# Optimization experiments

Hardware: AMD Instinct MI355X
Metric: run time of the kernel (lower is better)

## Reference

```python
import jax, jax.numpy as jnp
from jax import lax
import numpy as np

SUB_SAMPLE = 16
NMS_THRESH = 0.7
N_PRE_NMS = 2000
N_POST_NMS = 300
MIN_SIZE = 16.0
SCALE = 1.0
NEG_INF = -1e9


def _anchor_base(base=16.0, ratios=(0.5, 1.0, 2.0), scales=(8.0, 16.0, 32.0)):
    r = np.asarray(ratios, np.float32)[:, None]
    s = np.asarray(scales, np.float32)[None, :]
    h = base * s * np.sqrt(r)
    w = base * s * np.sqrt(1.0 / r)
    ctr = base / 2.0
    ab = np.stack([ctr - h / 2, ctr - w / 2, ctr + h / 2, ctr + w / 2], axis=-1)
    return ab.reshape(-1, 4).astype(np.float32)  # [9,4] (y1,x1,y2,x2)


def _decode(anchors, locs):
    # anchors/locs: [K,4]; loc2bbox
    ah = anchors[:, 2] - anchors[:, 0]
    aw = anchors[:, 3] - anchors[:, 1]
    acy = anchors[:, 0] + 0.5 * ah
    acx = anchors[:, 1] + 0.5 * aw
    dy, dx, dh, dw = locs[:, 0], locs[:, 1], locs[:, 2], locs[:, 3]
    cy = dy * ah + acy
    cx = dx * aw + acx
    h = jnp.exp(dh) * ah
    w = jnp.exp(dw) * aw
    return jnp.stack([cy - 0.5 * h, cx - 0.5 * w, cy + 0.5 * h, cx + 0.5 * w], axis=-1)


def _pairwise_iou(b):
    # b: [P,4] y1x1y2x2
    tl = jnp.maximum(b[:, None, :2], b[None, :, :2])
    br = jnp.minimum(b[:, None, 2:], b[None, :, 2:])
    wh = jnp.clip(br - tl, 0.0)
    inter = wh[..., 0] * wh[..., 1]
    area = (b[:, 2] - b[:, 0]) * (b[:, 3] - b[:, 1])
    return inter / (area[:, None] + area[None, :] - inter + 1e-9)


def _propose(locs_i, fg_i, anchors, img_h, img_w):
    boxes = _decode(anchors, locs_i)
    boxes = jnp.stack([
        jnp.clip(boxes[:, 0], 0.0, img_h), jnp.clip(boxes[:, 1], 0.0, img_w),
        jnp.clip(boxes[:, 2], 0.0, img_h), jnp.clip(boxes[:, 3], 0.0, img_w)], axis=-1)
    hs = boxes[:, 2] - boxes[:, 0]
    ws = boxes[:, 3] - boxes[:, 1]
    ok = (hs >= MIN_SIZE * SCALE) & (ws >= MIN_SIZE * SCALE)
    sc = jnp.where(ok, fg_i, NEG_INF)
    top_sc, order = lax.top_k(sc, N_PRE_NMS)  # sorted desc by score
    b = boxes[order]
    iou = _pairwise_iou(b)
    idx = jnp.arange(N_PRE_NMS)
    sup = (iou > NMS_THRESH) & (idx[None, :] > idx[:, None])  # only suppress lower-scored
    keep0 = top_sc > NEG_INF / 2  # drop min-size-filtered padding

    def body(i, keep):
        return jnp.where(keep[i], keep & ~sup[i], keep)

    keep = lax.fori_loop(0, N_PRE_NMS, body, keep0)
    prio = jnp.where(keep, idx, N_PRE_NMS)
    sel = jnp.argsort(prio)[:N_POST_NMS]  # kept boxes first, score order preserved
    valid = keep[sel]
    rois = jnp.where(valid[:, None], b[sel], 0.0)
    return rois, valid


def setup_inputs() -> dict:
    key = jax.random.key(0)
    ks = jax.random.split(key, 6)
    N, C, Hf, Wf = 8, 512, 64, 64
    std = 0.01  # normal_init(0, 0.01)
    return {
        "x": jax.random.normal(ks[0], (N, C, Hf, Wf), jnp.float32),
        "conv1_w": jax.random.normal(ks[1], (512, 512, 3, 3), jnp.float32) * std,
        "conv1_b": jnp.zeros((512,), jnp.float32),
        "score_w": jax.random.normal(ks[2], (18, 512, 1, 1), jnp.float32) * std,
        "score_b": jnp.zeros((18,), jnp.float32),
        "loc_w": jax.random.normal(ks[3], (36, 512, 1, 1), jnp.float32) * std,
        "loc_b": jnp.zeros((36,), jnp.float32),
        "img_h": 1024,
        "img_w": 1024,
    }


def reference(x, conv1_w, conv1_b, score_w, score_b, loc_w, loc_b, img_h, img_w):
    N, _, Hf, Wf = x.shape
    ab = jnp.asarray(_anchor_base())
    A = ab.shape[0]
    sy = jnp.arange(Hf, dtype=jnp.float32) * SUB_SAMPLE
    sx = jnp.arange(Wf, dtype=jnp.float32) * SUB_SAMPLE
    Y, X = jnp.meshgrid(sy, sx, indexing='ij')
    shifts = jnp.stack([Y, X, Y, X], axis=-1).reshape(-1, 4)
    anchors = (shifts[:, None, :] + ab[None, :, :]).reshape(-1, 4)  # [H*W*A,4]

    hidden = jax.nn.relu(
        lax.conv_general_dilated(x, conv1_w, (1, 1), 'SAME',
                                 dimension_numbers=('NCHW', 'OIHW', 'NCHW'))
        + conv1_b[None, :, None, None])
    scores = jnp.einsum('nchw,oc->nhwo', hidden, score_w[:, :, 0, 0]) + score_b  # [N,H,W,2A]
    locs = jnp.einsum('nchw,oc->nhwo', hidden, loc_w[:, :, 0, 0]) + loc_b        # [N,H,W,4A]

    rpn_locs = locs.reshape(N, -1, 4)
    rpn_scores = scores.reshape(N, -1, 2)
    soft = jax.nn.softmax(scores.reshape(N, Hf, Wf, A, 2), axis=-1)
    rpn_fg = soft[..., 1].reshape(N, -1)

    fh = jnp.float32(img_h)
    fw = jnp.float32(img_w)
    rois, valid = jax.vmap(lambda l, s: _propose(l, s, anchors, fh, fw))(rpn_locs, rpn_fg)
    roi_indices = jnp.repeat(jnp.arange(N, dtype=jnp.int32), N_POST_NMS)
    return rpn_locs, rpn_scores, rois.reshape(-1, 4), roi_indices, anchors
```

## Files before the change

kernel.cpp:

```cpp
#include <hip/hip_runtime.h>
#include <math.h>

typedef unsigned int u32;
typedef unsigned long long u64;

#define NIMG 8
#define CIN 512
#define COUT 512
#define HF 64
#define WF 64
#define NPOS 4096
#define NANCH 36864
#define NPRE 2000
#define NPOST 300
#define SUPW 32

#define OUT_LOCS   0
#define OUT_SCORES 1179648
#define OUT_ROIS   1769472
#define OUT_ROIIDX 1779072
#define OUT_ANCH   1781472

__device__ __forceinline__ u32 fkey(float f) {
  u32 s = __float_as_uint(f);
  return (s & 0x80000000u) ? ~s : (s | 0x80000000u);
}
__device__ __forceinline__ float unkey(u32 u) {
  u32 s = (u & 0x80000000u) ? (u ^ 0x80000000u) : ~u;
  return __uint_as_float(s);
}
__device__ __forceinline__ void anchor_at(int hq, int wq, int a,
                                          float& a0, float& a1, float& a2, float& a3) {
  const float ratios[3] = {0.5f, 1.0f, 2.0f};
  const float scales[3] = {8.0f, 16.0f, 32.0f};
  float r = ratios[a / 3];
  float s = scales[a % 3];
  float hh = __fmul_rn(__fmul_rn(16.0f, s), sqrtf(r));
  float ww = __fmul_rn(__fmul_rn(16.0f, s), sqrtf(1.0f / r));
  float ab0 = __fsub_rn(8.0f, __fmul_rn(0.5f, hh));
  float ab1 = __fsub_rn(8.0f, __fmul_rn(0.5f, ww));
  float ab2 = __fadd_rn(8.0f, __fmul_rn(0.5f, hh));
  float ab3 = __fadd_rn(8.0f, __fmul_rn(0.5f, ww));
  float y = (float)(hq * 16);
  float x = (float)(wq * 16);
  a0 = __fadd_rn(y, ab0);
  a1 = __fadd_rn(x, ab1);
  a2 = __fadd_rn(y, ab2);
  a3 = __fadd_rn(x, ab3);
}
__device__ __forceinline__ u64 shfl_u64(u64 v, int src) {
  u32 lo = (u32)v, hi = (u32)(v >> 32);
  lo = __shfl(lo, src, 64);
  hi = __shfl(hi, src, 64);
  return ((u64)hi << 32) | (u64)lo;
}

__global__ __launch_bounds__(256) void k_prep_small(const float* __restrict__ sw,
                                                    const float* __restrict__ lw,
                                                    float* __restrict__ wt54,
                                                    float* __restrict__ out) {
  int i = blockIdx.x * 256 + threadIdx.x;
  if (i < 512 * 56) {
    int c = i / 56, o = i % 56;
    float v = 0.0f;
    if (o < 18) v = sw[o * 512 + c];
    else if (o < 54) v = lw[(o - 18) * 512 + c];
    wt54[i] = v;
  }
  if (i < NANCH) {
    int pos = i / 9, a = i % 9;
    float a0, a1, a2, a3;
    anchor_at(pos >> 6, pos & 63, a, a0, a1, a2, a3);
    float* dst = out + OUT_ANCH + (size_t)i * 4;
    dst[0] = a0; dst[1] = a1; dst[2] = a2; dst[3] = a3;
  }
  if (i < NIMG * NPOST) out[OUT_ROIIDX + i] = (float)(i / NPOST);
}

__global__ __launch_bounds__(256) void k_transpose_w(const float* __restrict__ w,
                                                     float* __restrict__ wt) {
  int o = blockIdx.x * 256 + threadIdx.x;
  if (o >= COUT * CIN * 9) return;
  int co = o & 511;
  int r = o >> 9;
  int tap = r % 9;
  int ci = r / 9;
  wt[o] = w[((size_t)co * CIN + ci) * 9 + tap];
}

#define TCI 4
__global__ __launch_bounds__(256, 2) void k_conv_fast(const float* __restrict__ x,
                                                      const float* __restrict__ wt,
                                                      const float* __restrict__ bias,
                                                      float* __restrict__ hidden) {
  __shared__ float in_lds[TCI][34][36];
  __shared__ float w_lds[TCI][9][32];
  const int tid = threadIdx.x;
  const int n  = blockIdx.x >> 2;
  const int h0 = ((blockIdx.x >> 1) & 1) * 32;
  const int w0 = (blockIdx.x & 1) * 32;
  const int co0 = blockIdx.y * 32;
  const int pix = tid & 63, cg = tid >> 6;
  const int py = (pix >> 3) * 4, px = (pix & 7) * 4;
  const float* xn = x + (size_t)n * CIN * NPOS;
  float acc[16][8] = {};

  for (int ci0 = 0; ci0 < CIN; ci0 += TCI) {
    for (int idx = tid; idx < TCI * 34 * 34; idx += 256) {
      int w = idx % 34;
      int r = (idx / 34) % 34;
      int c = idx / (34 * 34);
      int gh = h0 + r - 1, gw = w0 + w - 1;
      float v = 0.0f;
      if (gh >= 0 && gh < HF && gw >= 0 && gw < WF)
        v = xn[(size_t)(ci0 + c) * NPOS + gh * WF + gw];
      in_lds[c][r][w] = v;
    }
    for (int idx = tid; idx < TCI * 9 * 32; idx += 256) {
      int co = idx & 31;
      int tap = (idx >> 5) % 9;
      int c = idx / (9 * 32);
      w_lds[c][tap][co] = wt[((size_t)(ci0 + c) * 9 + tap) * COUT + co0 + co];
    }
    __syncthreads();
    #pragma unroll 1
    for (int c = 0; c < TCI; ++c) {
      float p[6][6];
      #pragma unroll
      for (int r = 0; r < 6; ++r)
        #pragma unroll
        for (int q = 0; q < 6; ++q)
          p[r][q] = in_lds[c][py + r][px + q];
      #pragma unroll
      for (int kh = 0; kh < 3; ++kh) {
        #pragma unroll
        for (int kw = 0; kw < 3; ++kw) {
          const float4 wa = *(const float4*)&w_lds[c][kh * 3 + kw][cg * 8];
          const float4 wb = *(const float4*)&w_lds[c][kh * 3 + kw][cg * 8 + 4];
          #pragma unroll
          for (int r = 0; r < 4; ++r) {
            #pragma unroll
            for (int q = 0; q < 4; ++q) {
              const float a = p[r + kh][q + kw];
              acc[r * 4 + q][0] = fmaf(a, wa.x, acc[r * 4 + q][0]);
              acc[r * 4 + q][1] = fmaf(a, wa.y, acc[r * 4 + q][1]);
              acc[r * 4 + q][2] = fmaf(a, wa.z, acc[r * 4 + q][2]);
              acc[r * 4 + q][3] = fmaf(a, wa.w, acc[r * 4 + q][3]);
              acc[r * 4 + q][4] = fmaf(a, wb.x, acc[r * 4 + q][4]);
              acc[r * 4 + q][5] = fmaf(a, wb.y, acc[r * 4 + q][5]);
              acc[r * 4 + q][6] = fmaf(a, wb.z, acc[r * 4 + q][6]);
              acc[r * 4 + q][7] = fmaf(a, wb.w, acc[r * 4 + q][7]);
            }
          }
        }
      }
    }
    __syncthreads();
  }
  #pragma unroll
  for (int co = 0; co < 8; ++co) {
    const float b = bias[co0 + cg * 8 + co];
    float* dst = hidden + ((size_t)(n * COUT + co0 + cg * 8 + co)) * NPOS;
    #pragma unroll
    for (int r = 0; r < 4; ++r) {
      float4 v;
      v.x = fmaxf(acc[r * 4 + 0][co] + b, 0.0f);
      v.y = fmaxf(acc[r * 4 + 1][co] + b, 0.0f);
      v.z = fmaxf(acc[r * 4 + 2][co] + b, 0.0f);
      v.w = fmaxf(acc[r * 4 + 3][co] + b, 0.0f);
      *(float4*)&dst[(h0 + py + r) * WF + (w0 + px)] = v;
    }
  }
}

__global__ __launch_bounds__(256) void k_heads(const float* __restrict__ hidden,
                                               const float* __restrict__ wt54,
                                               const float* __restrict__ sb,
                                               const float* __restrict__ lb,
                                               const int* __restrict__ ihp,
                                               const int* __restrict__ iwp,
                                               float* __restrict__ out,
                                               float4* __restrict__ boxes_all,
                                               u64* __restrict__ k64) {
  const int n = blockIdx.y;
  const int hw = blockIdx.x * 256 + threadIdx.x;
  const float* hid = hidden + (size_t)n * CIN * NPOS + hw;
  float acc[54];
  #pragma unroll
  for (int o = 0; o < 54; ++o) acc[o] = 0.0f;
  #pragma unroll 4
  for (int c = 0; c < CIN; ++c) {
    float hv = hid[(size_t)c * NPOS];
    const float* wrow = wt54 + c * 56;
    #pragma unroll
    for (int o = 0; o < 54; ++o) acc[o] = fmaf(hv, wrow[o], acc[o]);
  }
  float sc18[18];
  #pragma unroll
  for (int o = 0; o < 18; ++o) sc18[o] = __fadd_rn(acc[o], sb[o]);
  float lc36[36];
  #pragma unroll
  for (int o = 0; o < 36; ++o) lc36[o] = __fadd_rn(acc[18 + o], lb[o]);
  {
    float* dst = out + OUT_SCORES + ((size_t)n * NPOS + hw) * 18;
    #pragma unroll
    for (int q = 0; q < 9; ++q) *(float2*)&dst[q * 2] = make_float2(sc18[2 * q], sc18[2 * q + 1]);
  }
  {
    float* dst = out + OUT_LOCS + ((size_t)n * NPOS + hw) * 36;
    #pragma unroll
    for (int q = 0; q < 9; ++q)
      *(float4*)&dst[q * 4] = make_float4(lc36[4 * q], lc36[4 * q + 1], lc36[4 * q + 2], lc36[4 * q + 3]);
  }
  const float fh = (float)ihp[0];
  const float fw = (float)iwp[0];
  const int hq = hw >> 6, wq2 = hw & 63;
  #pragma unroll
  for (int a = 0; a < 9; ++a) {
    float a0, a1, a2, a3;
    anchor_at(hq, wq2, a, a0, a1, a2, a3);
    float ah = __fsub_rn(a2, a0), aw = __fsub_rn(a3, a1);
    float acy = __fadd_rn(a0, __fmul_rn(0.5f, ah));
    float acx = __fadd_rn(a1, __fmul_rn(0.5f, aw));
    float dy = lc36[4 * a], dx = lc36[4 * a + 1], dh = lc36[4 * a + 2], dw = lc36[4 * a + 3];
    float cy = __fadd_rn(__fmul_rn(dy, ah), acy);
    float cx = __fadd_rn(__fmul_rn(dx, aw), acx);
    float hh = __fmul_rn(expf(dh), ah);
    float ww = __fmul_rn(expf(dw), aw);
    float y1 = __fsub_rn(cy, __fmul_rn(0.5f, hh));
    float x1 = __fsub_rn(cx, __fmul_rn(0.5f, ww));
    float y2 = __fadd_rn(cy, __fmul_rn(0.5f, hh));
    float x2 = __fadd_rn(cx, __fmul_rn(0.5f, ww));
    y1 = fminf(fmaxf(y1, 0.0f), fh);
    y2 = fminf(fmaxf(y2, 0.0f), fh);
    x1 = fminf(fmaxf(x1, 0.0f), fw);
    x2 = fminf(fmaxf(x2, 0.0f), fw);
    float hs = __fsub_rn(y2, y1), wsz = __fsub_rn(x2, x1);
    bool ok = (hs >= 16.0f) && (wsz >= 16.0f);
    float l0 = sc18[2 * a], l1 = sc18[2 * a + 1];
    float m = fmaxf(l0, l1);
    float e0 = expf(__fsub_rn(l0, m));
    float e1 = expf(__fsub_rn(l1, m));
    float fg = __fdiv_rn(e1, __fadd_rn(e0, e1));
    float sc = ok ? fg : -1000000000.0f;
    int idx = hw * 9 + a;
    boxes_all[(size_t)n * NANCH + idx] = make_float4(y1, x1, y2, x2);
    k64[(size_t)n * NANCH + idx] = ((u64)(~fkey(sc)) << 16) | (u32)idx;
  }
}

__global__ __launch_bounds__(1024) void k_topk(const u64* __restrict__ k64_all,
                                               const float4* __restrict__ boxes_all,
                                               float4* __restrict__ boxes_sorted,
                                               float* __restrict__ sc_sorted) {
  const int b = blockIdx.x;
  const int tid = threadIdx.x;
  const u64* kb = k64_all + (size_t)b * NANCH;
  __shared__ u32 hist[4096];
  __shared__ u32 coarse[1024];
  __shared__ u64 sortbuf[2048];
  __shared__ u32 sh_bucket, sh_before, sh_cnt;
  u64 prefix = 0ull;
  u32 rank = NPRE;
  for (int pass = 0; pass < 4; ++pass) {
    const int shift = 36 - 12 * pass;
    for (int i = tid; i < 4096; i += 1024) hist[i] = 0;
    __syncthreads();
    for (int i = tid; i < NANCH; i += 1024) {
      u64 k = kb[i];
      if ((k >> (shift + 12)) == prefix)
        atomicAdd(&hist[(u32)((k >> shift) & 4095ull)], 1u);
    }
    __syncthreads();
    u32 s = hist[4 * tid] + hist[4 * tid + 1] + hist[4 * tid + 2] + hist[4 * tid + 3];
    coarse[tid] = s;
    __syncthreads();
    for (int off = 1; off < 1024; off <<= 1) {
      u32 v = (tid >= off) ? coarse[tid - off] : 0u;
      __syncthreads();
      coarse[tid] += v;
      __syncthreads();
    }
    u32 lo = (tid == 0) ? 0u : coarse[tid - 1];
    u32 hi = coarse[tid];
    if (lo < rank && rank <= hi) {
      u32 c = lo;
      #pragma unroll
      for (int q = 0; q < 4; ++q) {
        u32 nb = c + hist[4 * tid + q];
        if (c < rank && rank <= nb) { sh_bucket = 4 * tid + q; sh_before = c; break; }
        c = nb;
      }
    }
    __syncthreads();
    prefix = (prefix << 12) | (u64)sh_bucket;
    rank -= sh_before;
    __syncthreads();
  }
  const u64 Kstar = prefix;
  if (tid == 0) sh_cnt = 0;
  __syncthreads();
  for (int i = tid; i < NANCH; i += 1024) {
    u64 k = kb[i];
    if (k <= Kstar) {
      u32 p = atomicAdd(&sh_cnt, 1u);
      if (p < 2048) sortbuf[p] = k;
    }
  }
  __syncthreads();
  u32 cnt = sh_cnt;
  for (int i = tid; i < 2048; i += 1024)
    if (i >= (int)cnt) sortbuf[i] = ~0ull;
  __syncthreads();
  for (int kk = 2; kk <= 2048; kk <<= 1) {
    for (int j = kk >> 1; j > 0; j >>= 1) {
      int i1 = 2 * j * (tid / j) + (tid % j);
      int i2 = i1 + j;
      bool up = ((i1 & kk) == 0);
      u64 va = sortbuf[i1], vb = sortbuf[i2];
      if ((va > vb) == up) { sortbuf[i1] = vb; sortbuf[i2] = va; }
      __syncthreads();
    }
  }
  for (int i = tid; i < NPRE; i += 1024) {
    u64 k = sortbuf[i];
    u32 idx = (u32)(k & 0xFFFFull);
    boxes_sorted[(size_t)b * NPRE + i] = boxes_all[(size_t)b * NANCH + idx];
    sc_sorted[(size_t)b * NPRE + i] = unkey(~(u32)(k >> 16));
  }
}

__global__ __launch_bounds__(64) void k_supmask(const float4* __restrict__ boxes_sorted,
                                                u64* __restrict__ sup) {
  const int b = blockIdx.z;
  const int i = blockIdx.x * 64 + threadIdx.x;
  const int j0 = blockIdx.y * 64;
  __shared__ float4 bj[64];
  int jg = j0 + threadIdx.x;
  bj[threadIdx.x] = (jg < NPRE) ? boxes_sorted[(size_t)b * NPRE + jg] : make_float4(0, 0, 0, 0);
  __syncthreads();
  if (i >= NPRE) return;
  float4 bi = boxes_sorted[(size_t)b * NPRE + i];
  float ai = __fmul_rn(__fsub_rn(bi.z, bi.x), __fsub_rn(bi.w, bi.y));
  u64 m = 0;
  for (int q = 0; q < 64; ++q) {
    int j = j0 + q;
    float4 bb = bj[q];
    float ty = fmaxf(bi.x, bb.x);
    float tx = fmaxf(bi.y, bb.y);
    float by = fminf(bi.z, bb.z);
    float bx = fminf(bi.w, bb.w);
    float ih2 = fmaxf(__fsub_rn(by, ty), 0.0f);
    float iw2 = fmaxf(__fsub_rn(bx, tx), 0.0f);
    float inter = __fmul_rn(ih2, iw2);
    float aj = __fmul_rn(__fsub_rn(bb.z, bb.x), __fsub_rn(bb.w, bb.y));
    float den = __fadd_rn(__fsub_rn(__fadd_rn(ai, aj), inter), 1e-9f);
    float iou = __fdiv_rn(inter, den);
    if (iou > 0.7f && j > i && j < NPRE) m |= (1ull << q);
  }
  sup[((size_t)b * NPRE + i) * SUPW + blockIdx.y] = m;
}

__global__ __launch_bounds__(64) void k_nms(const u64* __restrict__ sup,
                                            const float* __restrict__ sc_sorted,
                                            const float4* __restrict__ boxes_sorted,
                                            float* __restrict__ rois) {
  const int b = blockIdx.x;
  const int lane = threadIdx.x;
  __shared__ float sc[NPRE];
  for (int i = lane; i < NPRE; i += 64) sc[i] = sc_sorted[(size_t)b * NPRE + i];
  __syncthreads();
  const u64* supb = sup + (size_t)b * NPRE * SUPW;
  const float* bs = (const float*)(boxes_sorted + (size_t)b * NPRE);
  float* rb = rois + (size_t)b * NPOST * 4;
  u64 removed = 0ull;
  int kc = 0;
  for (int i = 0; i < NPRE; ++i) {
    int w = i >> 6;
    u64 rw = shfl_u64(removed, w);
    bool kept = (((rw >> (i & 63)) & 1ull) == 0ull) && (sc[i] > -5.0e8f);
    if (kept) {
      if (lane < 4) rb[(size_t)kc * 4 + lane] = bs[(size_t)i * 4 + lane];
      ++kc;
      if (kc >= NPOST) break;
      if (lane < 32) removed |= supb[(size_t)i * SUPW + lane];
    }
  }
  for (int z = lane; z < (NPOST - kc) * 4; z += 64) rb[(size_t)kc * 4 + z] = 0.0f;
}

extern "C" void kernel_launch(void* const* d_in, const int* in_sizes, int n_in,
                              void* d_out, int out_size, void* d_ws, size_t ws_size,
                              hipStream_t stream) {
  const float* x  = (const float*)d_in[0];
  const float* w1 = (const float*)d_in[1];
  const float* b1 = (const float*)d_in[2];
  const float* sw = (const float*)d_in[3];
  const float* sb = (const float*)d_in[4];
  const float* lw = (const float*)d_in[5];
  const float* lb = (const float*)d_in[6];
  const int* ih   = (const int*)d_in[7];
  const int* iw   = (const int*)d_in[8];
  float* out = (float*)d_out;
  char* ws = (char*)d_ws;
  (void)in_sizes; (void)n_in; (void)out_size; (void)ws_size;

  float* hidden       = (float*)(ws + 0);
  float* wt           = (float*)(ws + 67108864ull);
  float* wt54         = (float*)(ws + 76546048ull);
  float4* boxes_all   = (float4*)(ws + 67108864ull);
  u64*   k64          = (u64*)  (ws + 71827456ull);
  float4* boxes_sorted= (float4*)(ws + 0);
  float* sc_sorted    = (float*)(ws + 262144ull);
  u64*   sup          = (u64*)  (ws + 327680ull);

  k_transpose_w<<<9216, 256, 0, stream>>>(w1, wt);
  k_prep_small<<<144, 256, 0, stream>>>(sw, lw, wt54, out);
  k_conv_fast<<<dim3(32, 16), 256, 0, stream>>>(x, wt, b1, hidden);
  k_heads<<<dim3(16, 8), 256, 0, stream>>>(hidden, wt54, sb, lb, ih, iw, out, boxes_all, k64);
  k_topk<<<8, 1024, 0, stream>>>(k64, boxes_all, boxes_sorted, sc_sorted);
  k_supmask<<<dim3(32, 32, 8), 64, 0, stream>>>(boxes_sorted, sup);
  k_nms<<<8, 64, 0, stream>>>(sup, sc_sorted, boxes_sorted, out + OUT_ROIS);
}
```

Measured before the change: 2.538 ms.

## Pre-pad input and double-buffer LDS tiles in conv with vectorized loads

Adds a kernel that writes a zero-padded copy of the input so the conv can load its halo tiles with unconditional float4 loads. The new conv kernel double-buffers input and weight tiles in LDS, prefetching the next channel group into registers while computing the current one, so there is one barrier per iteration instead of two. This costs an extra pass over the input (about 140MB of workspace traffic) and more LDS and registers. The new path runs only if the workspace is large enough; otherwise it falls back to the old conv.

```diff
diff --git a/kernel.cpp b/kernel.cpp
--- a/kernel.cpp
+++ b/kernel.cpp
@@ -88,7 +88,143 @@
   wt[o] = w[((size_t)co * CIN + ci) * 9 + tap];
 }
 
+__global__ __launch_bounds__(256) void k_padx(const float* __restrict__ x,
+                                              float* __restrict__ xp) {
+  int idx = blockIdx.x * 256 + threadIdx.x;
+  if (idx >= 8 * 512 * 66 * 68) return;
+  int wp = idx % 68;
+  int rest = idx / 68;
+  int hp = rest % 66;
+  int nc = rest / 66;
+  float v = 0.0f;
+  if (hp >= 1 && hp <= 64 && wp >= 1 && wp <= 64)
+    v = x[(size_t)nc * NPOS + (hp - 1) * 64 + (wp - 1)];
+  xp[idx] = v;
+}
+
 #define TCI 4
+#define INQ 1224
+#define WQ  288
+__global__ __launch_bounds__(256, 2) void k_conv_db(const float* __restrict__ xp,
+                                                    const float* __restrict__ wt,
+                                                    const float* __restrict__ bias,
+                                                    float* __restrict__ hidden) {
+  __shared__ float in_s[2][TCI * 34 * 36];
+  __shared__ float w_s[2][TCI * 9 * 32];
+  const int tid = threadIdx.x;
+  const int n  = blockIdx.x >> 2;
+  const int h0 = ((blockIdx.x >> 1) & 1) * 32;
+  const int w0 = (blockIdx.x & 1) * 32;
+  const int co0 = blockIdx.y * 32;
+  const int pix = tid & 63, cg = tid >> 6;
+  const int py = (pix >> 3) * 4, px = (pix & 7) * 4;
+
+  const float* gin[5];
+  int lin[5];
+  #pragma unroll
+  for (int k = 0; k < 5; ++k) {
+    int qq = tid + k * 256; qq = qq < INQ ? qq : INQ - 1;
+    int c = qq / 306, rem = qq % 306;
+    int rr = rem / 9, wq = rem % 9;
+    gin[k] = xp + ((size_t)(n * 512 + c) * 66 + (h0 + rr)) * 68 + w0 + wq * 4;
+    lin[k] = (c * 34 + rr) * 36 + wq * 4;
+  }
+  const float* gw[2];
+  int lw[2];
+  #pragma unroll
+  for (int k = 0; k < 2; ++k) {
+    int qq = tid + k * 256; qq = qq < WQ ? qq : WQ - 1;
+    int c = qq / 72, rem = qq % 72;
+    int tap = rem / 8, l = rem % 8;
+    gw[k] = wt + ((size_t)c * 9 + tap) * 512 + co0 + l * 4;
+    lw[k] = (c * 9 + tap) * 32 + l * 4;
+  }
+
+  float acc[16][8] = {};
+  float4 s[5], sw_[2];
+
+  #pragma unroll
+  for (int k = 0; k < 5; ++k) { s[k] = *(const float4*)gin[k]; gin[k] += TCI * 66 * 68; }
+  #pragma unroll
+  for (int k = 0; k < 2; ++k) { sw_[k] = *(const float4*)gw[k]; gw[k] += TCI * 9 * 512; }
+  #pragma unroll
+  for (int k = 0; k < 5; ++k) *(float4*)&in_s[0][lin[k]] = s[k];
+  #pragma unroll
+  for (int k = 0; k < 2; ++k) *(float4*)&w_s[0][lw[k]] = sw_[k];
+  __syncthreads();
+
+  #pragma unroll 1
+  for (int t = 0; t < 128; ++t) {
+    const int b = t & 1;
+    if (t < 127) {
+      #pragma unroll
+      for (int k = 0; k < 5; ++k) { s[k] = *(const float4*)gin[k]; gin[k] += TCI * 66 * 68; }
+      #pragma unroll
+      for (int k = 0; k < 2; ++k) { sw_[k] = *(const float4*)gw[k]; gw[k] += TCI * 9 * 512; }
+    }
+    const float* ib = &in_s[b][0];
+    const float* wb_ = &w_s[b][0];
+    #pragma unroll 1
+    for (int c = 0; c < TCI; ++c) {
+      const float* cb = ib + (c * 34 + py) * 36 + px;
+      float p[6][6];
+      #pragma unroll
+      for (int rr = 0; rr < 6; ++rr) {
+        const float4 v4 = *(const float4*)(cb + rr * 36);
+        const float2 v2 = *(const float2*)(cb + rr * 36 + 4);
+        p[rr][0] = v4.x; p[rr][1] = v4.y; p[rr][2] = v4.z; p[rr][3] = v4.w;
+        p[rr][4] = v2.x; p[rr][5] = v2.y;
+      }
+      #pragma unroll
+      for (int kh = 0; kh < 3; ++kh) {
+        #pragma unroll
+        for (int kw = 0; kw < 3; ++kw) {
+          const float* wp_ = wb_ + (c * 9 + kh * 3 + kw) * 32 + cg * 8;
+          const float4 wa = *(const float4*)wp_;
+          const float4 wb2 = *(const float4*)(wp_ + 4);
+          #pragma unroll
+          for (int r = 0; r < 4; ++r) {
+            #pragma unroll
+            for (int q = 0; q < 4; ++q) {
+              const float a = p[r + kh][q + kw];
+              acc[r * 4 + q][0] = fmaf(a, wa.x, acc[r * 4 + q][0]);
+              acc[r * 4 + q][1] = fmaf(a, wa.y, acc[r * 4 + q][1]);
+              acc[r * 4 + q][2] = fmaf(a, wa.z, acc[r * 4 + q][2]);
+              acc[r * 4 + q][3] = fmaf(a, wa.w, acc[r * 4 + q][3]);
+              acc[r * 4 + q][4] = fmaf(a, wb2.x, acc[r * 4 + q][4]);
+              acc[r * 4 + q][5] = fmaf(a, wb2.y, acc[r * 4 + q][5]);
+              acc[r * 4 + q][6] = fmaf(a, wb2.z, acc[r * 4 + q][6]);
+              acc[r * 4 + q][7] = fmaf(a, wb2.w, acc[r * 4 + q][7]);
+            }
+          }
+        }
+      }
+    }
+    if (t < 127) {
+      #pragma unroll
+      for (int k = 0; k < 5; ++k) *(float4*)&in_s[b ^ 1][lin[k]] = s[k];
+      #pragma unroll
+      for (int k = 0; k < 2; ++k) *(float4*)&w_s[b ^ 1][lw[k]] = sw_[k];
+    }
+    __syncthreads();
+  }
+
+  #pragma unroll
+  for (int co = 0; co < 8; ++co) {
+    const float b = bias[co0 + cg * 8 + co];
+    float* dst = hidden + ((size_t)(n * COUT + co0 + cg * 8 + co)) * NPOS;
+    #pragma unroll
+    for (int r = 0; r < 4; ++r) {
+      float4 v;
+      v.x = fmaxf(acc[r * 4 + 0][co] + b, 0.0f);
+      v.y = fmaxf(acc[r * 4 + 1][co] + b, 0.0f);
+      v.z = fmaxf(acc[r * 4 + 2][co] + b, 0.0f);
+      v.w = fmaxf(acc[r * 4 + 3][co] + b, 0.0f);
+      *(float4*)&dst[(h0 + py + r) * WF + (w0 + px)] = v;
+    }
+  }
+}
+
 __global__ __launch_bounds__(256, 2) void k_conv_fast(const float* __restrict__ x,
                                                       const float* __restrict__ wt,
                                                       const float* __restrict__ bias,
@@ -104,7 +240,6 @@
   const int py = (pix >> 3) * 4, px = (pix & 7) * 4;
   const float* xn = x + (size_t)n * CIN * NPOS;
   float acc[16][8] = {};
-
   for (int ci0 = 0; ci0 < CIN; ci0 += TCI) {
     for (int idx = tid; idx < TCI * 34 * 34; idx += 256) {
       int w = idx % 34;
@@ -403,22 +538,43 @@
   const int* iw   = (const int*)d_in[8];
   float* out = (float*)d_out;
   char* ws = (char*)d_ws;
-  (void)in_sizes; (void)n_in; (void)out_size; (void)ws_size;
-
-  float* hidden       = (float*)(ws + 0);
-  float* wt           = (float*)(ws + 67108864ull);
-  float* wt54         = (float*)(ws + 76546048ull);
-  float4* boxes_all   = (float4*)(ws + 67108864ull);
-  u64*   k64          = (u64*)  (ws + 71827456ull);
-  float4* boxes_sorted= (float4*)(ws + 0);
-  float* sc_sorted    = (float*)(ws + 262144ull);
-  u64*   sup          = (u64*)  (ws + 327680ull);
-
-  k_transpose_w<<<9216, 256, 0, stream>>>(w1, wt);
-  k_prep_small<<<144, 256, 0, stream>>>(sw, lw, wt54, out);
-  k_conv_fast<<<dim3(32, 16), 256, 0, stream>>>(x, wt, b1, hidden);
-  k_heads<<<dim3(16, 8), 256, 0, stream>>>(hidden, wt54, sb, lb, ih, iw, out, boxes_all, k64);
-  k_topk<<<8, 1024, 0, stream>>>(k64, boxes_all, boxes_sorted, sc_sorted);
-  k_supmask<<<dim3(32, 32, 8), 64, 0, stream>>>(boxes_sorted, sup);
-  k_nms<<<8, 64, 0, stream>>>(sup, sc_sorted, boxes_sorted, out + OUT_ROIS);
-}
+  (void)in_sizes; (void)n_in; (void)out_size;
+
+  const size_t NEED = 150192128ull;
+  float* hidden = (float*)ws;
+  if (ws_size >= NEED) {
+    float* xp   = (float*)(ws + 67108864ull);
+    float* wt   = (float*)(ws + 140640256ull);
+    float* wt54 = (float*)(ws + 150077440ull);
+    float4* boxes_all    = (float4*)(ws + 67108864ull);
+    u64*   k64           = (u64*)  (ws + 71827456ull);
+    float4* boxes_sorted = (float4*)(ws + 74186752ull);
+    float* sc_sorted     = (float*)(ws + 74442752ull);
+    u64*   sup           = (u64*)  (ws + 74506752ull);
+
+    k_transpose_w<<<9216, 256, 0, stream>>>(w1, wt);
+    k_prep_small<<<144, 256, 0, stream>>>(sw, lw, wt54, out);
+    k_padx<<<71808, 256, 0, stream>>>(x, xp);
+    k_conv_db<<<dim3(32, 16), 256, 0, stream>>>(xp, wt, b1, hidden);
+    k_heads<<<dim3(16, 8), 256, 0, stream>>>(hidden, wt54, sb, lb, ih, iw, out, boxes_all, k64);
+    k_topk<<<8, 1024, 0, stream>>>(k64, boxes_all, boxes_sorted, sc_sorted);
+    k_supmask<<<dim3(32, 32, 8), 64, 0, stream>>>(boxes_sorted, sup);
+    k_nms<<<8, 64, 0, stream>>>(sup, sc_sorted, boxes_sorted, out + OUT_ROIS);
+  } else {
+    float* wt           = (float*)(ws + 67108864ull);
+    float* wt54         = (float*)(ws + 76546048ull);
+    float4* boxes_all   = (float4*)(ws + 67108864ull);
+    u64*   k64          = (u64*)  (ws + 71827456ull);
+    float4* boxes_sorted= (float4*)(ws + 0);
+    float* sc_sorted    = (float*)(ws + 262144ull);
+    u64*   sup          = (u64*)  (ws + 327680ull);
+
+    k_transpose_w<<<9216, 256, 0, stream>>>(w1, wt);
+    k_prep_small<<<144, 256, 0, stream>>>(sw, lw, wt54, out);
+    k_conv_fast<<<dim3(32, 16), 256, 0, stream>>>(x, wt, b1, hidden);
+    k_heads<<<dim3(16, 8), 256, 0, stream>>>(hidden, wt54, sb, lb, ih, iw, out, boxes_all, k64);
+    k_topk<<<8, 1024, 0, stream>>>(k64, boxes_all, boxes_sorted, sc_sorted);
+    k_supmask<<<dim3(32, 32, 8), 64, 0, stream>>>(boxes_sorted, sup);
+    k_nms<<<8, 64, 0, stream>>>(sup, sc_sorted, boxes_sorted, out + OUT_ROIS);
+  }
+}
```

Result: slower. 3.892 ms (+53.4%).
